# Kernel tuning notes

Measured on AMD Instinct MI355X. Metric: run time of the kernel, lower is better.

## Reference

```python
import jax, jax.numpy as jnp
import numpy as np

T, B, F = 1024, 32, 2048
H, C = 64, 101


def setup_inputs() -> dict:
    key = jax.random.key(0)
    ks = jax.random.split(key, 7)
    s = 0.02
    return {
        "x": jax.random.normal(ks[0], (T, B, F), dtype=jnp.float32),
        "W_ih": jax.random.normal(ks[1], (4 * H, F), dtype=jnp.float32) * s,
        "W_hh": jax.random.normal(ks[2], (4 * H, H), dtype=jnp.float32) * s,
        "b_ih": jax.random.normal(ks[3], (4 * H,), dtype=jnp.float32) * s,
        "b_hh": jax.random.normal(ks[4], (4 * H,), dtype=jnp.float32) * s,
        "W_lin": jax.random.normal(ks[5], (C, H), dtype=jnp.float32) * s,
        "b_lin": jax.random.normal(ks[6], (C,), dtype=jnp.float32) * s,
    }


def reference(x, W_ih, W_hh, b_ih, b_hh, W_lin, b_lin):
    # Sequential LSTMCell over T timesteps, PyTorch gate order (i, f, g, o).
    # Precompute the input projection for all timesteps in one big GEMM;
    # only the tiny [B,H]x[H,4H] recurrent matmul stays inside the scan.
    x_proj = jnp.einsum('tbf,gf->tbg', x, W_ih) + b_ih + b_hh  # [T, B, 4H]

    h0 = jnp.zeros((B, H), dtype=x.dtype)
    c0 = jnp.zeros((B, H), dtype=x.dtype)

    def step(carry, xp_t):
        h, c = carry
        gates = xp_t + h @ W_hh.T  # [B, 4H]
        i, f, g, o = jnp.split(gates, 4, axis=-1)
        c_new = jax.nn.sigmoid(f) * c + jax.nn.sigmoid(i) * jnp.tanh(g)
        h_new = jax.nn.sigmoid(o) * jnp.tanh(c_new)
        return (h_new, c_new), None

    (h_T, _), _ = jax.lax.scan(step, (h0, c0), x_proj)
    # Original module returns only the final step's linear output.
    return h_T @ W_lin.T + b_lin  # [B, C]
```

## Files before the change

### kernel.cpp

```cpp
#include <hip/hip_runtime.h>
#include <hip/hip_bf16.h>
#include <math.h>

#define T_STEPS 1024
#define B_SZ 32
#define F_SZ 2048
#define H_SZ 64
#define G4 256
#define C_SZ 101

typedef __bf16 bf16x8 __attribute__((ext_vector_type(8)));
typedef unsigned short u16x8 __attribute__((ext_vector_type(8)));
typedef unsigned short u16x4 __attribute__((ext_vector_type(4)));
typedef float f32x4 __attribute__((ext_vector_type(4)));
typedef _Float16 f16x4 __attribute__((ext_vector_type(4)));
typedef _Float16 f16x8 __attribute__((ext_vector_type(8)));

__device__ __forceinline__ void split_bf16(float f, unsigned short& h,
                                           unsigned short& l) {
  unsigned u = __builtin_bit_cast(unsigned, f);
  unsigned rh = (u + 0x7FFFu + ((u >> 16) & 1u)) >> 16;
  h = (unsigned short)rh;
  float d = f - __builtin_bit_cast(float, rh << 16);
  unsigned ud = __builtin_bit_cast(unsigned, d);
  l = (unsigned short)((ud + 0x7FFFu + ((ud >> 16) & 1u)) >> 16);
}

__device__ __forceinline__ float sigm_f(float x) {
  return __builtin_amdgcn_rcpf(1.f + __expf(-x));
}
__device__ __forceinline__ float tanh_f(float x) {
  return 2.f * __builtin_amdgcn_rcpf(1.f + __expf(-2.f * x)) - 1.f;
}

__device__ __forceinline__ float sel4(float a0, float a1, float a2, float a3,
                                      bool k1, bool k2) {
  const float t0 = k1 ? a1 : a0;
  const float t1 = k1 ? a3 : a2;
  return k2 ? t1 : t0;
}

#define REP8(M) M(0) M(1) M(2) M(3) M(4) M(5) M(6) M(7)
#define REP16(M) M(0) M(1) M(2) M(3) M(4) M(5) M(6) M(7) \
                 M(8) M(9) M(10) M(11) M(12) M(13) M(14) M(15)

__global__ __launch_bounds__(256) void presplit_w(
    const float* __restrict__ W, unsigned short* __restrict__ hi,
    unsigned short* __restrict__ lo) {
  const int idx = (blockIdx.x * 256 + threadIdx.x) * 4;
  float4 v = *(const float4*)(W + idx);
  unsigned short h0, l0, h1, l1, h2, l2, h3, l3;
  split_bf16(v.x, h0, l0);
  split_bf16(v.y, h1, l1);
  split_bf16(v.z, h2, l2);
  split_bf16(v.w, h3, l3);
  *(u16x4*)(hi + idx) = u16x4{h0, h1, h2, h3};
  *(u16x4*)(lo + idx) = u16x4{l0, l1, l2, l3};
}

__global__ __launch_bounds__(256) void whh_to_f16(
    const float* __restrict__ W, _Float16* __restrict__ o) {
  const int idx = (blockIdx.x * 256 + threadIdx.x) * 4;
  float4 v = *(const float4*)(W + idx);
  f16x4 r = {(_Float16)v.x, (_Float16)v.y, (_Float16)v.z, (_Float16)v.w};
  *(f16x4*)(o + idx) = r;
}

#define BM 128
#define BK 32
#define LDSP 40

__global__ __launch_bounds__(512) void xproj_mfma(
    const float* __restrict__ x, const unsigned short* __restrict__ Whi_g,
    const unsigned short* __restrict__ Wlo_g, const float* __restrict__ b_ih,
    const float* __restrict__ b_hh, float* __restrict__ xproj) {
  __shared__ alignas(16) unsigned short Xhi[BM][LDSP];
  __shared__ alignas(16) unsigned short Xlo[BM][LDSP];
  __shared__ alignas(16) unsigned short Whi[G4][LDSP];
  __shared__ alignas(16) unsigned short Wlo[G4][LDSP];

  const int tid = threadIdx.x;
  const int lane = tid & 63;
  const int wave = tid >> 6;
  const int wm = wave >> 2;
  const int wn = wave & 3;
  const size_t R0 = (size_t)blockIdx.x * BM;

  const int xr = tid >> 2;
  const int xs = (tid & 3) * 8;
  const int wr = tid >> 1;
  const int wsg = (tid & 1) * 16;

  const float* xbase = x + (R0 + xr) * (size_t)F_SZ + xs;
  const unsigned short* whb = Whi_g + (size_t)wr * F_SZ + wsg;
  const unsigned short* wlb = Wlo_g + (size_t)wr * F_SZ + wsg;

  float4 xa = *(const float4*)(xbase + 0);
  float4 xb = *(const float4*)(xbase + 4);
  u16x8 wh0 = *(const u16x8*)(whb + 0);
  u16x8 wh1 = *(const u16x8*)(whb + 8);
  u16x8 wl0 = *(const u16x8*)(wlb + 0);
  u16x8 wl1 = *(const u16x8*)(wlb + 8);

  f32x4 acc[4][4] = {};

  const int ar = lane & 15;
  const int ak = (lane >> 4) * 8;

  for (int kt = 0; kt < F_SZ; kt += BK) {
    {
      float xf[8] = {xa.x, xa.y, xa.z, xa.w, xb.x, xb.y, xb.z, xb.w};
      u16x8 xh, xl;
#pragma unroll
      for (int i = 0; i < 8; ++i) {
        unsigned short h, l;
        split_bf16(xf[i], h, l);
        xh[i] = h;
        xl[i] = l;
      }
      *(u16x8*)&Xhi[xr][xs] = xh;
      *(u16x8*)&Xlo[xr][xs] = xl;
      *(u16x8*)&Whi[wr][wsg] = wh0;
      *(u16x8*)&Whi[wr][wsg + 8] = wh1;
      *(u16x8*)&Wlo[wr][wsg] = wl0;
      *(u16x8*)&Wlo[wr][wsg + 8] = wl1;
    }
    __syncthreads();

    const int ktn = (kt + BK < F_SZ) ? kt + BK : kt;
    xa = *(const float4*)(xbase + ktn + 0);
    xb = *(const float4*)(xbase + ktn + 4);
    wh0 = *(const u16x8*)(whb + ktn + 0);
    wh1 = *(const u16x8*)(whb + ktn + 8);
    wl0 = *(const u16x8*)(wlb + ktn + 0);
    wl1 = *(const u16x8*)(wlb + ktn + 8);

    bf16x8 Ah[4], Al[4], Bh[4], Bl[4];
#pragma unroll
    for (int fm = 0; fm < 4; ++fm) {
      const int row = wm * 64 + fm * 16 + ar;
      Ah[fm] = __builtin_bit_cast(bf16x8, *(const u16x8*)&Xhi[row][ak]);
      Al[fm] = __builtin_bit_cast(bf16x8, *(const u16x8*)&Xlo[row][ak]);
    }
#pragma unroll
    for (int fn = 0; fn < 4; ++fn) {
      const int col = wn * 64 + fn * 16 + ar;
      Bh[fn] = __builtin_bit_cast(bf16x8, *(const u16x8*)&Whi[col][ak]);
      Bl[fn] = __builtin_bit_cast(bf16x8, *(const u16x8*)&Wlo[col][ak]);
    }
#pragma unroll
    for (int fm = 0; fm < 4; ++fm) {
#pragma unroll
      for (int fn = 0; fn < 4; ++fn) {
        acc[fm][fn] = __builtin_amdgcn_mfma_f32_16x16x32_bf16(
            Ah[fm], Bh[fn], acc[fm][fn], 0, 0, 0);
        acc[fm][fn] = __builtin_amdgcn_mfma_f32_16x16x32_bf16(
            Ah[fm], Bl[fn], acc[fm][fn], 0, 0, 0);
        acc[fm][fn] = __builtin_amdgcn_mfma_f32_16x16x32_bf16(
            Al[fm], Bh[fn], acc[fm][fn], 0, 0, 0);
      }
    }
    __syncthreads();
  }

  const int cr = (lane >> 4) * 4;
  const int cc = lane & 15;
#pragma unroll
  for (int fn = 0; fn < 4; ++fn) {
    const int gj = wn * 64 + fn * 16 + cc;
    const float bias = b_ih[gj] + b_hh[gj];
#pragma unroll
    for (int fm = 0; fm < 4; ++fm) {
      const size_t gr = R0 + wm * 64 + fm * 16 + cr;
#pragma unroll
      for (int r = 0; r < 4; ++r) {
        xproj[(gr + r) * G4 + gj] = acc[fm][fn][r] + bias;
      }
    }
  }
}

__global__ __attribute__((amdgpu_flat_work_group_size(64, 64)))
__attribute__((amdgpu_waves_per_eu(1, 1))) void lstm_scan_mfma(
    const float* __restrict__ xproj, const _Float16* __restrict__ Whh16,
    float* __restrict__ hT) {
  const int b = blockIdx.x;
  const int l = threadIdx.x;
  const int kg8 = (l >> 4) * 8;
  const bool k1 = ((l >> 4) & 1) != 0;
  const bool k2 = ((l >> 4) & 2) != 0;

  __shared__ alignas(16) _Float16 hbuf[2][H_SZ];

  const _Float16* wb = Whh16 + (size_t)(l & 15) * H_SZ + kg8;
#define PINB(n)                                                               \
  f32x4 wB0_##n, wB1_##n;                                                     \
  {                                                                           \
    const _Float16* a0_##n = wb + (n) * (16 * H_SZ);                          \
    const _Float16* a1_##n = wb + (n) * (16 * H_SZ) + 32;                     \
    asm volatile("global_load_dwordx4 %0, %1, off" : "=v"(wB0_##n) : "v"(a0_##n)); \
    asm volatile("global_load_dwordx4 %0, %1, off" : "=v"(wB1_##n) : "v"(a1_##n)); \
  }
  REP16(PINB)
#undef PINB
  asm volatile("s_waitcnt vmcnt(0)" ::: "memory");

  f32x4 zq = {0.f, 0.f, 0.f, 0.f};
  asm volatile("" : "+v"(zq));

  hbuf[0][l] = (_Float16)0.f;
  float c = 0.f, hval = 0.f;
  int p = 0;

  const float* a_next = xproj + (size_t)b * G4 + l;
  const size_t step_off = (size_t)B_SZ * G4;

  float xi0, xf0, xg0, xo0, xi1, xf1, xg1, xo1;
  float xi2, xf2, xg2, xo2, xi3, xf3, xg3, xo3;

#define XLOAD(S, a)                                                     \
  asm volatile("global_load_dword %0, %4, off\n\t"                      \
               "global_load_dword %1, %4, off offset:256\n\t"           \
               "global_load_dword %2, %4, off offset:512\n\t"           \
               "global_load_dword %3, %4, off offset:768"               \
               : "=&v"(xi##S), "=&v"(xf##S), "=&v"(xg##S), "=&v"(xo##S) \
               : "v"(a));

  XLOAD(0, a_next) a_next += step_off;
  XLOAD(1, a_next) a_next += step_off;
  XLOAD(2, a_next) a_next += step_off;
  XLOAD(3, a_next) a_next += step_off;

  for (int it = 0; it < T_STEPS / 4; ++it) {
    const int tb = it * 4;

#define TILE(n)                                                               \
    f32x4 acc_##n;                                                            \
    acc_##n = __builtin_amdgcn_mfma_f32_16x16x32_f16(                         \
        hA0, __builtin_bit_cast(f16x8, wB0_##n), zq, 0, 0, 0);                \
    acc_##n = __builtin_amdgcn_mfma_f32_16x16x32_f16(                         \
        hA1, __builtin_bit_cast(f16x8, wB1_##n), acc_##n, 0, 0, 0);

#define SLOT(S)                                                               \
    {                                                                         \
                              \
      asm volatile("s_waitcnt vmcnt(12)"                                      \
                   : "+v"(xi##S), "+v"(xf##S), "+v"(xg##S), "+v"(xo##S));     \
        \
      const f16x8 hA0 = *(const f16x8*)&hbuf[p][kg8];                         \
      const f16x8 hA1 = *(const f16x8*)&hbuf[p][32 + kg8];                    \
      REP16(TILE)                                                             \
             \
      const float di = sel4(acc_0[0], acc_1[0], acc_2[0], acc_3[0], k1, k2);  \
      const float df = sel4(acc_4[0], acc_5[0], acc_6[0], acc_7[0], k1, k2);  \
      const float dg = sel4(acc_8[0], acc_9[0], acc_10[0], acc_11[0], k1, k2);\
      const float dq = sel4(acc_12[0], acc_13[0], acc_14[0], acc_15[0], k1, k2);\
      const float pi = xi##S + di;                                            \
      const float pf = xf##S + df;                                            \
      const float pg = xg##S + dg;                                            \
      const float po = xo##S + dq;                                            \
      c = sigm_f(pf) * c + sigm_f(pi) * tanh_f(pg);                           \
      hval = sigm_f(po) * tanh_f(c);                                          \
      hbuf[p ^ 1][l] = (_Float16)hval;                                        \
      p ^= 1;                                                                 \
         \
      XLOAD(S, a_next)                                                        \
      if (tb + (S) + 4 < T_STEPS - 1) a_next += step_off;                     \
    }

    SLOT(0)
    SLOT(1)
    SLOT(2)
    SLOT(3)

#undef SLOT
#undef TILE
  }
#undef XLOAD

  hT[b * H_SZ + l] = hval;
}

__global__ __launch_bounds__(128) void final_linear_kernel(
    const float* __restrict__ hT, const float* __restrict__ W_lin,
    const float* __restrict__ b_lin, float* __restrict__ out) {
  const int b = blockIdx.x;
  const int cc = threadIdx.x;

  __shared__ float h_l[H_SZ];
  if (threadIdx.x < H_SZ) h_l[threadIdx.x] = hT[b * H_SZ + threadIdx.x];
  __syncthreads();

  if (cc < C_SZ) {
    float acc = b_lin[cc];
    const float* wr = W_lin + (size_t)cc * H_SZ;
#pragma unroll
    for (int k = 0; k < H_SZ; ++k) acc += h_l[k] * wr[k];
    out[b * C_SZ + cc] = acc;
  }
}

extern "C" void kernel_launch(void* const* d_in, const int* in_sizes, int n_in,
                              void* d_out, int out_size, void* d_ws,
                              size_t ws_size, hipStream_t stream) {
  const float* x = (const float*)d_in[0];
  const float* W_ih = (const float*)d_in[1];
  const float* W_hh = (const float*)d_in[2];
  const float* b_ih = (const float*)d_in[3];
  const float* b_hh = (const float*)d_in[4];
  const float* W_lin = (const float*)d_in[5];
  const float* b_lin = (const float*)d_in[6];
  float* out = (float*)d_out;

  const size_t XP_BYTES = (size_t)T_STEPS * B_SZ * G4 * sizeof(float);
  float* xproj = (float*)d_ws;
  float* hT = (float*)((char*)d_ws + XP_BYTES);
  unsigned short* Whi_g = (unsigned short*)((char*)d_ws + XP_BYTES + 8192);
  unsigned short* Wlo_g = Whi_g + (size_t)G4 * F_SZ;
  _Float16* Whh16 = (_Float16*)(Wlo_g + (size_t)G4 * F_SZ);

  presplit_w<<<512, 256, 0, stream>>>(W_ih, Whi_g, Wlo_g);
  whh_to_f16<<<16, 256, 0, stream>>>(W_hh, Whh16);
  xproj_mfma<<<(T_STEPS * B_SZ) / BM, 512, 0, stream>>>(x, Whi_g, Wlo_g, b_ih,
                                                        b_hh, xproj);
  lstm_scan_mfma<<<B_SZ, 64, 0, stream>>>(xproj, Whh16, hT);
  final_linear_kernel<<<B_SZ, 128, 0, stream>>>(hT, W_lin, b_lin, out);
}
```

Before: 535.8 us.

## Fold log2e scaling into weights and xproj, split MFMA chains, defer waitcnt

Pre-scales W_hh and the input projection by log2(e), or 2*log2(e) for the g gate, so the recurrent step can call v_exp_f32 directly with a negated operand. The cell state is kept pre-scaled by 2*log2(e) so tanh(c) also reduces to one exp2 and one rcp. The two dependent MFMAs per tile become independent accumulators summed afterwards, and the xproj wait is moved after the MFMAs. The aim is to shorten the serial per-step latency chain. The trade-off is extra rounding from scaling before the fp16 conversion.

```diff
diff --git a/kernel.cpp b/kernel.cpp
--- a/kernel.cpp
+++ b/kernel.cpp
@@ -8,6 +8,8 @@
 #define H_SZ 64
 #define G4 256
 #define C_SZ 101
+
+#define LOG2E 1.4426950408889634f
 
 typedef __bf16 bf16x8 __attribute__((ext_vector_type(8)));
 typedef unsigned short u16x8 __attribute__((ext_vector_type(8)));
@@ -26,11 +28,13 @@
   l = (unsigned short)((ud + 0x7FFFu + ((ud >> 16) & 1u)) >> 16);
 }
 
-__device__ __forceinline__ float sigm_f(float x) {
-  return __builtin_amdgcn_rcpf(1.f + __expf(-x));
-}
-__device__ __forceinline__ float tanh_f(float x) {
-  return 2.f * __builtin_amdgcn_rcpf(1.f + __expf(-2.f * x)) - 1.f;
+__device__ __forceinline__ float exp2_neg(float x) {
+  float r;
+  asm("v_exp_f32 %0, -%1" : "=v"(r) : "v"(x));
+  return r;
+}
+__device__ __forceinline__ float sig2(float pp) {
+  return __builtin_amdgcn_rcpf(1.f + exp2_neg(pp));
 }
 
 __device__ __forceinline__ float sel4(float a0, float a1, float a2, float a3,
@@ -61,8 +65,12 @@
 __global__ __launch_bounds__(256) void whh_to_f16(
     const float* __restrict__ W, _Float16* __restrict__ o) {
   const int idx = (blockIdx.x * 256 + threadIdx.x) * 4;
+  const int row = idx >> 6;
+  const int gate = row >> 6;
+  const float s = (gate == 2) ? 2.f * LOG2E : LOG2E;
   float4 v = *(const float4*)(W + idx);
-  f16x4 r = {(_Float16)v.x, (_Float16)v.y, (_Float16)v.z, (_Float16)v.w};
+  f16x4 r = {(_Float16)(v.x * s), (_Float16)(v.y * s), (_Float16)(v.z * s),
+             (_Float16)(v.w * s)};
   *(f16x4*)(o + idx) = r;
 }
 
@@ -169,12 +177,13 @@
   for (int fn = 0; fn < 4; ++fn) {
     const int gj = wn * 64 + fn * 16 + cc;
     const float bias = b_ih[gj] + b_hh[gj];
+    const float scale = (gj >= 128 && gj < 192) ? 2.f * LOG2E : LOG2E;
 #pragma unroll
     for (int fm = 0; fm < 4; ++fm) {
       const size_t gr = R0 + wm * 64 + fm * 16 + cr;
 #pragma unroll
       for (int r = 0; r < 4; ++r) {
-        xproj[(gr + r) * G4 + gj] = acc[fm][fn][r] + bias;
+        xproj[(gr + r) * G4 + gj] = (acc[fm][fn][r] + bias) * scale;
       }
     }
   }
@@ -209,7 +218,7 @@
   asm volatile("" : "+v"(zq));
 
   hbuf[0][l] = (_Float16)0.f;
-  float c = 0.f, hval = 0.f;
+  float cq = 0.f, hval = 0.f;
   int p = 0;
 
   const float* a_next = xproj + (size_t)b * G4 + l;
@@ -235,32 +244,41 @@
     const int tb = it * 4;
 
 #define TILE(n)                                                               \
-    f32x4 acc_##n;                                                            \
-    acc_##n = __builtin_amdgcn_mfma_f32_16x16x32_f16(                         \
+    f32x4 accA_##n, accB_##n;                                                 \
+    accA_##n = __builtin_amdgcn_mfma_f32_16x16x32_f16(                        \
         hA0, __builtin_bit_cast(f16x8, wB0_##n), zq, 0, 0, 0);                \
-    acc_##n = __builtin_amdgcn_mfma_f32_16x16x32_f16(                         \
-        hA1, __builtin_bit_cast(f16x8, wB1_##n), acc_##n, 0, 0, 0);
+    accB_##n = __builtin_amdgcn_mfma_f32_16x16x32_f16(                        \
+        hA1, __builtin_bit_cast(f16x8, wB1_##n), zq, 0, 0, 0);
 
 #define SLOT(S)                                                               \
     {                                                                         \
-                              \
-      asm volatile("s_waitcnt vmcnt(12)"                                      \
-                   : "+v"(xi##S), "+v"(xf##S), "+v"(xg##S), "+v"(xo##S));     \
-        \
+                           \
       const f16x8 hA0 = *(const f16x8*)&hbuf[p][kg8];                         \
       const f16x8 hA1 = *(const f16x8*)&hbuf[p][32 + kg8];                    \
       REP16(TILE)                                                             \
-             \
-      const float di = sel4(acc_0[0], acc_1[0], acc_2[0], acc_3[0], k1, k2);  \
-      const float df = sel4(acc_4[0], acc_5[0], acc_6[0], acc_7[0], k1, k2);  \
-      const float dg = sel4(acc_8[0], acc_9[0], acc_10[0], acc_11[0], k1, k2);\
-      const float dq = sel4(acc_12[0], acc_13[0], acc_14[0], acc_15[0], k1, k2);\
+            \
+      asm volatile("s_waitcnt vmcnt(12)"                                      \
+                   : "+v"(xi##S), "+v"(xf##S), "+v"(xg##S), "+v"(xo##S));     \
+      const float di = sel4(accA_0[0], accA_1[0], accA_2[0], accA_3[0], k1, k2)   \
+                     + sel4(accB_0[0], accB_1[0], accB_2[0], accB_3[0], k1, k2);  \
+      const float df = sel4(accA_4[0], accA_5[0], accA_6[0], accA_7[0], k1, k2)   \
+                     + sel4(accB_4[0], accB_5[0], accB_6[0], accB_7[0], k1, k2);  \
+      const float dg = sel4(accA_8[0], accA_9[0], accA_10[0], accA_11[0], k1, k2) \
+                     + sel4(accB_8[0], accB_9[0], accB_10[0], accB_11[0], k1, k2);\
+      const float dq = sel4(accA_12[0], accA_13[0], accA_14[0], accA_15[0], k1, k2)   \
+                     + sel4(accB_12[0], accB_13[0], accB_14[0], accB_15[0], k1, k2);  \
       const float pi = xi##S + di;                                            \
       const float pf = xf##S + df;                                            \
       const float pg = xg##S + dg;                                            \
       const float po = xo##S + dq;                                            \
-      c = sigm_f(pf) * c + sigm_f(pi) * tanh_f(pg);                           \
-      hval = sigm_f(po) * tanh_f(c);                                          \
+      const float si = sig2(pi);                                              \
+      const float sf = sig2(pf);                                              \
+      const float so = sig2(po);                                              \
+      const float rg = sig2(pg);                                              \
+      const float gt = __builtin_fmaf(rg, 4.f * LOG2E, -2.f * LOG2E);         \
+      cq = __builtin_fmaf(sf, cq, si * gt);                                   \
+      const float tc = __builtin_fmaf(sig2(cq), 2.f, -1.f);                   \
+      hval = so * tc;                                                         \
       hbuf[p ^ 1][l] = (_Float16)hval;                                        \
       p ^= 1;                                                                 \
          \
```

Result: slower. 585.3 us (+9.2%).

## Switch input projection to single-pass fp16 MFMA and fuse weight conversion and final linear

Applied to the files above, without the earlier changes.

Replaces the three-pass bf16 hi/lo split GEMM for the input projection with a single fp16 MFMA pass. This cuts the matrix-core work and LDS traffic to roughly a third and removes the split arithmetic. The two weight-conversion kernels are merged into one launch, and the final linear layer is folded into the tail of the scan kernel, which saves two launches. The cost is precision: the GEMM now runs in fp16 with an fp32 accumulator instead of an emulated near-fp32 product, and x values round to fp16 with reduced mantissa.

```diff
diff --git a/kernel.cpp b/kernel.cpp
--- a/kernel.cpp
+++ b/kernel.cpp
@@ -9,21 +9,15 @@
 #define G4 256
 #define C_SZ 101
 
-typedef __bf16 bf16x8 __attribute__((ext_vector_type(8)));
 typedef unsigned short u16x8 __attribute__((ext_vector_type(8)));
 typedef unsigned short u16x4 __attribute__((ext_vector_type(4)));
 typedef float f32x4 __attribute__((ext_vector_type(4)));
 typedef _Float16 f16x4 __attribute__((ext_vector_type(4)));
 typedef _Float16 f16x8 __attribute__((ext_vector_type(8)));
 
-__device__ __forceinline__ void split_bf16(float f, unsigned short& h,
-                                           unsigned short& l) {
-  unsigned u = __builtin_bit_cast(unsigned, f);
-  unsigned rh = (u + 0x7FFFu + ((u >> 16) & 1u)) >> 16;
-  h = (unsigned short)rh;
-  float d = f - __builtin_bit_cast(float, rh << 16);
-  unsigned ud = __builtin_bit_cast(unsigned, d);
-  l = (unsigned short)((ud + 0x7FFFu + ((ud >> 16) & 1u)) >> 16);
+__device__ __forceinline__ unsigned short f2h(float f) {
+  _Float16 h = (_Float16)f;
+  return __builtin_bit_cast(unsigned short, h);
 }
 
 __device__ __forceinline__ float sigm_f(float x) {
@@ -40,44 +34,36 @@
   return k2 ? t1 : t0;
 }
 
-#define REP8(M) M(0) M(1) M(2) M(3) M(4) M(5) M(6) M(7)
 #define REP16(M) M(0) M(1) M(2) M(3) M(4) M(5) M(6) M(7) \
                  M(8) M(9) M(10) M(11) M(12) M(13) M(14) M(15)
 
-__global__ __launch_bounds__(256) void presplit_w(
-    const float* __restrict__ W, unsigned short* __restrict__ hi,
-    unsigned short* __restrict__ lo) {
-  const int idx = (blockIdx.x * 256 + threadIdx.x) * 4;
-  float4 v = *(const float4*)(W + idx);
-  unsigned short h0, l0, h1, l1, h2, l2, h3, l3;
-  split_bf16(v.x, h0, l0);
-  split_bf16(v.y, h1, l1);
-  split_bf16(v.z, h2, l2);
-  split_bf16(v.w, h3, l3);
-  *(u16x4*)(hi + idx) = u16x4{h0, h1, h2, h3};
-  *(u16x4*)(lo + idx) = u16x4{l0, l1, l2, l3};
-}
-
-__global__ __launch_bounds__(256) void whh_to_f16(
-    const float* __restrict__ W, _Float16* __restrict__ o) {
-  const int idx = (blockIdx.x * 256 + threadIdx.x) * 4;
-  float4 v = *(const float4*)(W + idx);
-  f16x4 r = {(_Float16)v.x, (_Float16)v.y, (_Float16)v.z, (_Float16)v.w};
-  *(f16x4*)(o + idx) = r;
+__global__ __launch_bounds__(256) void conv_w(
+    const float* __restrict__ Wih, const float* __restrict__ Whh,
+    _Float16* __restrict__ o_ih, _Float16* __restrict__ o_hh) {
+  const int bid = blockIdx.x;
+  if (bid < 512) {
+    const int idx = (bid * 256 + threadIdx.x) * 4;
+    float4 v = *(const float4*)(Wih + idx);
+    f16x4 r = {(_Float16)v.x, (_Float16)v.y, (_Float16)v.z, (_Float16)v.w};
+    *(f16x4*)(o_ih + idx) = r;
+  } else {
+    const int idx = ((bid - 512) * 256 + threadIdx.x) * 4;
+    float4 v = *(const float4*)(Whh + idx);
+    f16x4 r = {(_Float16)v.x, (_Float16)v.y, (_Float16)v.z, (_Float16)v.w};
+    *(f16x4*)(o_hh + idx) = r;
+  }
 }
 
 #define BM 128
 #define BK 32
 #define LDSP 40
 
-__global__ __launch_bounds__(512) void xproj_mfma(
-    const float* __restrict__ x, const unsigned short* __restrict__ Whi_g,
-    const unsigned short* __restrict__ Wlo_g, const float* __restrict__ b_ih,
-    const float* __restrict__ b_hh, float* __restrict__ xproj) {
-  __shared__ alignas(16) unsigned short Xhi[BM][LDSP];
-  __shared__ alignas(16) unsigned short Xlo[BM][LDSP];
-  __shared__ alignas(16) unsigned short Whi[G4][LDSP];
-  __shared__ alignas(16) unsigned short Wlo[G4][LDSP];
+__global__ __launch_bounds__(512) void xproj_f16(
+    const float* __restrict__ x, const _Float16* __restrict__ Wih16,
+    const float* __restrict__ b_ih, const float* __restrict__ b_hh,
+    float* __restrict__ xproj) {
+  __shared__ alignas(16) unsigned short Xf[BM][LDSP];
+  __shared__ alignas(16) unsigned short Wf[G4][LDSP];
 
   const int tid = threadIdx.x;
   const int lane = tid & 63;
@@ -92,15 +78,13 @@
   const int wsg = (tid & 1) * 16;
 
   const float* xbase = x + (R0 + xr) * (size_t)F_SZ + xs;
-  const unsigned short* whb = Whi_g + (size_t)wr * F_SZ + wsg;
-  const unsigned short* wlb = Wlo_g + (size_t)wr * F_SZ + wsg;
+  const unsigned short* wbase =
+      (const unsigned short*)Wih16 + (size_t)wr * F_SZ + wsg;
 
   float4 xa = *(const float4*)(xbase + 0);
   float4 xb = *(const float4*)(xbase + 4);
-  u16x8 wh0 = *(const u16x8*)(whb + 0);
-  u16x8 wh1 = *(const u16x8*)(whb + 8);
-  u16x8 wl0 = *(const u16x8*)(wlb + 0);
-  u16x8 wl1 = *(const u16x8*)(wlb + 8);
+  u16x8 wh0 = *(const u16x8*)(wbase + 0);
+  u16x8 wh1 = *(const u16x8*)(wbase + 8);
 
   f32x4 acc[4][4] = {};
 
@@ -109,55 +93,44 @@
 
   for (int kt = 0; kt < F_SZ; kt += BK) {
     {
-      float xf[8] = {xa.x, xa.y, xa.z, xa.w, xb.x, xb.y, xb.z, xb.w};
-      u16x8 xh, xl;
-#pragma unroll
-      for (int i = 0; i < 8; ++i) {
-        unsigned short h, l;
-        split_bf16(xf[i], h, l);
-        xh[i] = h;
-        xl[i] = l;
-      }
-      *(u16x8*)&Xhi[xr][xs] = xh;
-      *(u16x8*)&Xlo[xr][xs] = xl;
-      *(u16x8*)&Whi[wr][wsg] = wh0;
-      *(u16x8*)&Whi[wr][wsg + 8] = wh1;
-      *(u16x8*)&Wlo[wr][wsg] = wl0;
-      *(u16x8*)&Wlo[wr][wsg + 8] = wl1;
+      u16x8 xh;
+      xh[0] = f2h(xa.x);
+      xh[1] = f2h(xa.y);
+      xh[2] = f2h(xa.z);
+      xh[3] = f2h(xa.w);
+      xh[4] = f2h(xb.x);
+      xh[5] = f2h(xb.y);
+      xh[6] = f2h(xb.z);
+      xh[7] = f2h(xb.w);
+      *(u16x8*)&Xf[xr][xs] = xh;
+      *(u16x8*)&Wf[wr][wsg] = wh0;
+      *(u16x8*)&Wf[wr][wsg + 8] = wh1;
     }
     __syncthreads();
 
     const int ktn = (kt + BK < F_SZ) ? kt + BK : kt;
     xa = *(const float4*)(xbase + ktn + 0);
     xb = *(const float4*)(xbase + ktn + 4);
-    wh0 = *(const u16x8*)(whb + ktn + 0);
-    wh1 = *(const u16x8*)(whb + ktn + 8);
-    wl0 = *(const u16x8*)(wlb + ktn + 0);
-    wl1 = *(const u16x8*)(wlb + ktn + 8);
-
-    bf16x8 Ah[4], Al[4], Bh[4], Bl[4];
+    wh0 = *(const u16x8*)(wbase + ktn + 0);
+    wh1 = *(const u16x8*)(wbase + ktn + 8);
+
+    f16x8 A[4], Bv[4];
 #pragma unroll
     for (int fm = 0; fm < 4; ++fm) {
       const int row = wm * 64 + fm * 16 + ar;
-      Ah[fm] = __builtin_bit_cast(bf16x8, *(const u16x8*)&Xhi[row][ak]);
-      Al[fm] = __builtin_bit_cast(bf16x8, *(const u16x8*)&Xlo[row][ak]);
+      A[fm] = __builtin_bit_cast(f16x8, *(const u16x8*)&Xf[row][ak]);
     }
 #pragma unroll
     for (int fn = 0; fn < 4; ++fn) {
       const int col = wn * 64 + fn * 16 + ar;
-      Bh[fn] = __builtin_bit_cast(bf16x8, *(const u16x8*)&Whi[col][ak]);
-      Bl[fn] = __builtin_bit_cast(bf16x8, *(const u16x8*)&Wlo[col][ak]);
+      Bv[fn] = __builtin_bit_cast(f16x8, *(const u16x8*)&Wf[col][ak]);
     }
 #pragma unroll
     for (int fm = 0; fm < 4; ++fm) {
 #pragma unroll
       for (int fn = 0; fn < 4; ++fn) {
-        acc[fm][fn] = __builtin_amdgcn_mfma_f32_16x16x32_bf16(
-            Ah[fm], Bh[fn], acc[fm][fn], 0, 0, 0);
-        acc[fm][fn] = __builtin_amdgcn_mfma_f32_16x16x32_bf16(
-            Ah[fm], Bl[fn], acc[fm][fn], 0, 0, 0);
-        acc[fm][fn] = __builtin_amdgcn_mfma_f32_16x16x32_bf16(
-            Al[fm], Bh[fn], acc[fm][fn], 0, 0, 0);
+        acc[fm][fn] = __builtin_amdgcn_mfma_f32_16x16x32_f16(
+            A[fm], Bv[fn], acc[fm][fn], 0, 0, 0);
       }
     }
     __syncthreads();
@@ -183,7 +156,8 @@
 __global__ __attribute__((amdgpu_flat_work_group_size(64, 64)))
 __attribute__((amdgpu_waves_per_eu(1, 1))) void lstm_scan_mfma(
     const float* __restrict__ xproj, const _Float16* __restrict__ Whh16,
-    float* __restrict__ hT) {
+    const float* __restrict__ W_lin, const float* __restrict__ b_lin,
+    float* __restrict__ out) {
   const int b = blockIdx.x;
   const int l = threadIdx.x;
   const int kg8 = (l >> 4) * 8;
@@ -191,6 +165,7 @@
   const bool k2 = ((l >> 4) & 2) != 0;
 
   __shared__ alignas(16) _Float16 hbuf[2][H_SZ];
+  __shared__ alignas(16) float hfin[H_SZ];
 
   const _Float16* wb = Whh16 + (size_t)(l & 15) * H_SZ + kg8;
 #define PINB(n)                                                               \
@@ -278,25 +253,31 @@
   }
 #undef XLOAD
 
-  hT[b * H_SZ + l] = hval;
-}
-
-__global__ __launch_bounds__(128) void final_linear_kernel(
-    const float* __restrict__ hT, const float* __restrict__ W_lin,
-    const float* __restrict__ b_lin, float* __restrict__ out) {
-  const int b = blockIdx.x;
-  const int cc = threadIdx.x;
-
-  __shared__ float h_l[H_SZ];
-  if (threadIdx.x < H_SZ) h_l[threadIdx.x] = hT[b * H_SZ + threadIdx.x];
-  __syncthreads();
-
-  if (cc < C_SZ) {
-    float acc = b_lin[cc];
-    const float* wr = W_lin + (size_t)cc * H_SZ;
-#pragma unroll
-    for (int k = 0; k < H_SZ; ++k) acc += h_l[k] * wr[k];
-    out[b * C_SZ + cc] = acc;
+  hfin[l] = hval;
+
+  {
+    float acc0 = b_lin[l];
+    const float* wr0 = W_lin + (size_t)l * H_SZ;
+#pragma unroll
+    for (int k = 0; k < 16; ++k) {
+      const float4 w = *(const float4*)(wr0 + 4 * k);
+      const float4 h = *(const float4*)&hfin[4 * k];
+      acc0 += w.x * h.x + w.y * h.y + w.z * h.z + w.w * h.w;
+    }
+    out[b * C_SZ + l] = acc0;
+
+    const int c1 = l + 64;
+    if (c1 < C_SZ) {
+      float acc1 = b_lin[c1];
+      const float* wr1 = W_lin + (size_t)c1 * H_SZ;
+#pragma unroll
+      for (int k = 0; k < 16; ++k) {
+        const float4 w = *(const float4*)(wr1 + 4 * k);
+        const float4 h = *(const float4*)&hfin[4 * k];
+        acc1 += w.x * h.x + w.y * h.y + w.z * h.z + w.w * h.w;
+      }
+      out[b * C_SZ + c1] = acc1;
+    }
   }
 }
 
@@ -314,15 +295,11 @@
 
   const size_t XP_BYTES = (size_t)T_STEPS * B_SZ * G4 * sizeof(float);
   float* xproj = (float*)d_ws;
-  float* hT = (float*)((char*)d_ws + XP_BYTES);
-  unsigned short* Whi_g = (unsigned short*)((char*)d_ws + XP_BYTES + 8192);
-  unsigned short* Wlo_g = Whi_g + (size_t)G4 * F_SZ;
-  _Float16* Whh16 = (_Float16*)(Wlo_g + (size_t)G4 * F_SZ);
-
-  presplit_w<<<512, 256, 0, stream>>>(W_ih, Whi_g, Wlo_g);
-  whh_to_f16<<<16, 256, 0, stream>>>(W_hh, Whh16);
-  xproj_mfma<<<(T_STEPS * B_SZ) / BM, 512, 0, stream>>>(x, Whi_g, Wlo_g, b_ih,
-                                                        b_hh, xproj);
-  lstm_scan_mfma<<<B_SZ, 64, 0, stream>>>(xproj, Whh16, hT);
-  final_linear_kernel<<<B_SZ, 128, 0, stream>>>(hT, W_lin, b_lin, out);
-}
+  _Float16* Wih16 = (_Float16*)((char*)d_ws + XP_BYTES);
+  _Float16* Whh16 = Wih16 + (size_t)G4 * F_SZ;
+
+  conv_w<<<528, 256, 0, stream>>>(W_ih, W_hh, Wih16, Whh16);
+  xproj_f16<<<(T_STEPS * B_SZ) / BM, 512, 0, stream>>>(x, Wih16, b_ih, b_hh,
+                                                       xproj);
+  lstm_scan_mfma<<<B_SZ, 64, 0, stream>>>(xproj, Whh16, W_lin, b_lin, out);
+}
```

Measured after the change: 484.2 us. 9.6% less time.
